# Performance work log

Hardware: AMD Instinct MI355X
Metric: run time of the kernel (lower is better)

## Reference

```python
import jax, jax.numpy as jnp
import numpy as np

HEADS = 16
HEAD_DIM = 64


def _attn(q, k, v):
    # q: [..., Q, h, d], k/v: [..., K, h, d]  (non-causal SDPA, scale 1/sqrt(d))
    scale = 1.0 / np.sqrt(HEAD_DIM).astype(np.float32)
    s = jnp.einsum('...qhd,...khd->...hqk', q, k) * scale
    p = jax.nn.softmax(s, axis=-1)
    return jnp.einsum('...hqk,...khd->...qhd', p, v)


def setup_inputs() -> dict:
    key = jax.random.key(0)
    k0, k1, k2 = jax.random.split(key, 3)
    B, T, H, W, D = 4, 32, 16, 16, 1024
    inner = HEADS * HEAD_DIM
    x = jax.random.normal(k0, (B, T, H, W, D), jnp.float32)
    Wqkv = jax.random.normal(k1, (D, 3 * inner), jnp.float32) / np.sqrt(D)
    Wout = jax.random.normal(k2, (inner, D), jnp.float32) / np.sqrt(inner)
    bout = jnp.zeros((D,), jnp.float32)
    return {"x": x, "Wqkv": Wqkv, "Wout": Wout, "bout": bout, "reference_length": 3}


def reference(x, Wqkv, Wout, bout, reference_length):
    B, T, H, W, D = x.shape
    length = reference_length + 1
    n = T // length            # n_frames (chunks)
    S = H * W                  # tokens per frame
    h, d = HEADS, HEAD_DIM

    qkv = jnp.einsum('bthwD,De->bthwe', x, Wqkv)
    q, k, v = jnp.split(qkv, 3, axis=-1)

    def rs(t):  # -> [B, n, length, S, h, d]
        return t.reshape(B, n, length, S, h, d)

    qr, kr, vr = rs(q), rs(k), rs(v)

    # non-last chunks: query = first frame of chunk, keys/values = remaining r frames
    q_pre = qr[:, :-1, 0]                                             # [B, n-1, S, h, d]
    k_pre = kr[:, :-1, 1:].reshape(B, n - 1, reference_length * S, h, d)
    v_pre = vr[:, :-1, 1:].reshape(B, n - 1, reference_length * S, h, d)
    o_pre = _attn(q_pre, k_pre, v_pre).reshape(B, n - 1, H, W, h * d)

    # last chunk: all `length` frames are queries, keys/values = frames 1..length-1
    q_last = qr[:, -1].reshape(B, length * S, h, d)
    k_last = kr[:, -1, 1:].reshape(B, reference_length * S, h, d)
    v_last = vr[:, -1, 1:].reshape(B, reference_length * S, h, d)
    o_last = _attn(q_last, k_last, v_last).reshape(B, length, H, W, h * d)

    o = jnp.concatenate([o_pre, o_last], axis=1)  # [B, n-1+length, H, W, inner]
    return jnp.einsum('bthwe,eD->bthwD', o, Wout) + bout
```

## Files before the change

### kernel.cpp

```cpp
#include <hip/hip_runtime.h>
#include <hip/hip_bf16.h>

typedef __bf16 bf16;
typedef __bf16 bf16x8 __attribute__((ext_vector_type(8)));
typedef float  f32x4  __attribute__((ext_vector_type(4)));
typedef float  f32x4v __attribute__((ext_vector_type(4)));
typedef unsigned int u32x4 __attribute__((ext_vector_type(4)));
typedef unsigned short u16x4 __attribute__((ext_vector_type(4)));

#define DEV __device__ __forceinline__

DEV void gload_lds16(const bf16* g, bf16* l) {
    __builtin_amdgcn_global_load_lds(
        (__attribute__((address_space(1))) void*)g,
        (__attribute__((address_space(3))) void*)l, 16, 0, 0);
}

DEV bf16x8 as_bf(u32x4 v) { return __builtin_bit_cast(bf16x8, v); }

DEV f32x4 mfma16(bf16x8 a, bf16x8 b, f32x4 c) {
    return __builtin_amdgcn_mfma_f32_16x16x32_bf16(a, b, c, 0, 0, 0);
}

DEV int cvtpk(float lo, float hi) {
    int r;
    asm("v_cvt_pk_bf16_f32 %0, %1, %2" : "=v"(r) : "v"(lo), "v"(hi));
    return r;
}

constexpr int D_   = 1024;
constexpr int S_   = 256;
constexpr int TOUT = 11;
constexpr int MQ   = 4 * TOUT * S_;
constexpr int MKV  = 4 * 8 * 3 * S_;
constexpr int KVL  = 768;

constexpr int PB_WQKV = 768;
constexpr int PB_WOUT = 256;
constexpr int PB_GQ   = MQ  * 128 / 256;
constexpr int PB_GKV  = MKV * 128 / 256;
constexpr int PB_TOT  = PB_WQKV + PB_WOUT + PB_GQ + PB_GKV;

__global__ void prep(const float* __restrict__ x,
                     const float* __restrict__ Wqkv,
                     const float* __restrict__ Wout,
                     bf16* __restrict__ Aq, bf16* __restrict__ Akv,
                     bf16* __restrict__ Wqkv_t, bf16* __restrict__ Wout_t)
{
    __shared__ float T[64][65];
    const int tid = threadIdx.x;
    int wg = blockIdx.x;

    if (wg < PB_WQKV + PB_WOUT) {
        const float* W; bf16* Wt; int N, bid2;
        if (wg < PB_WQKV) { W = Wqkv; Wt = Wqkv_t; N = 3072; bid2 = wg; }
        else              { W = Wout; Wt = Wout_t; N = 1024; bid2 = wg - PB_WQKV; }
        const int kt = bid2 & 15, nt = bid2 >> 4;
        const int k0 = kt * 64, n0 = nt * 64;
        for (int i = 0; i < 16; ++i) {
            const int e = i * 256 + tid;
            const int kk = e >> 6, nn = e & 63;
            T[nn][kk] = W[(size_t)(k0 + kk) * N + n0 + nn];
        }
        __syncthreads();
        for (int i = 0; i < 16; ++i) {
            const int e = i * 256 + tid;
            const int n = e >> 6, kk = e & 63;
            Wt[(size_t)(n0 + n) * 1024 + k0 + kk] = (bf16)T[n][kk];
        }
        return;
    }
    wg -= PB_WQKV + PB_WOUT;

    int row, part;
    const float* src;
    bf16* dst;
    if (wg < PB_GQ) {
        const int idx = wg * 256 + tid;
        row = idx >> 7; part = idx & 127;
        const int b    = row / (TOUT * S_);
        const int r2   = row - b * (TOUT * S_);
        const int tout = r2 >> 8;
        const int s    = r2 & 255;
        const int tx   = tout < 7 ? tout * 4 : 28 + (tout - 7);
        src = x + ((size_t)((b * 32 + tx) * S_ + s)) * D_ + part * 8;
        dst = Aq + (size_t)row * D_ + part * 8;
    } else {
        const int idx = (wg - PB_GQ) * 256 + tid;
        row = idx >> 7; part = idx & 127;
        const int b  = row / 6144;
        const int r2 = row - b * 6144;
        const int c  = r2 / KVL;
        const int j  = r2 - c * KVL;
        const int f  = 1 + (j >> 8);
        const int s  = j & 255;
        const int tx = c * 4 + f;
        src = x + ((size_t)((b * 32 + tx) * S_ + s)) * D_ + part * 8;
        dst = Akv + (size_t)row * D_ + part * 8;
    }
    f32x4v v0 = *(const f32x4v*)src;
    f32x4v v1 = *(const f32x4v*)(src + 4);
    bf16x8 o;
    o[0]=(bf16)v0[0]; o[1]=(bf16)v0[1]; o[2]=(bf16)v0[2]; o[3]=(bf16)v0[3];
    o[4]=(bf16)v1[0]; o[5]=(bf16)v1[1]; o[6]=(bf16)v1[2]; o[7]=(bf16)v1[3];
    *(bf16x8*)dst = o;
}

#define PH_MID() do { \
    __builtin_amdgcn_s_barrier(); \
    asm volatile("s_waitcnt lgkmcnt(0)" ::: "memory"); \
    __builtin_amdgcn_sched_barrier(0); \
    __builtin_amdgcn_s_setprio(1); \
} while(0)

#define PH_END() do { \
    __builtin_amdgcn_s_setprio(0); \
    __builtin_amdgcn_sched_barrier(0); \
    __builtin_amdgcn_s_barrier(); \
} while(0)

#define VM6() asm volatile("s_waitcnt vmcnt(6)" ::: "memory")

#define STAGE_A(bufc, half, tile) do { \
    const bf16* s0_ = pA + (size_t)(half) * 64 * 1024 + (tile) * 64; \
    bf16* d0_ = ldsA + (bufc) * 16384 + (half) * 8192; \
    gload_lds16(s0_, d0_); \
    gload_lds16(s0_ + (size_t)128 * 1024, d0_ + 4096); \
} while(0)

#define STAGE_B(bufc, half, tile) do { \
    const bf16* s0_ = pB + (size_t)(half) * 32 * 1024 + (tile) * 64; \
    bf16* d0_ = ldsB + (bufc) * 16384 + (half) * 8192; \
    gload_lds16(s0_, d0_); \
    gload_lds16(s0_ + (size_t)128 * 1024, d0_ + 4096); \
} while(0)

#define LDA(bufc, mh) do { \
    const bf16* p_ = sm + (bufc) * 16384 + (mh) * 8192; \
    _Pragma("unroll") \
    for (int j_ = 0; j_ < 4; ++j_) { \
        a[j_][0] = *(const u32x4*)(p_ + j_ * 1024 + eA0); \
        a[j_][1] = *(const u32x4*)(p_ + j_ * 1024 + eA1); \
    } \
} while(0)

#define LDB(bufc, nh) do { \
    const bf16* p_ = sm + 32768 + (bufc) * 16384 + (nh) * 8192; \
    _Pragma("unroll") \
    for (int j_ = 0; j_ < 2; ++j_) { \
        b[(nh)*2 + j_][0] = *(const u32x4*)(p_ + j_ * 1024 + eB0); \
        b[(nh)*2 + j_][1] = *(const u32x4*)(p_ + j_ * 1024 + eB1); \
    } \
} while(0)

#define MM(mh, nh) do { \
    _Pragma("unroll") \
    for (int j_ = 0; j_ < 4; ++j_) { \
        _Pragma("unroll") \
        for (int i_ = 0; i_ < 2; ++i_) { \
            f32x4 c_ = acc[(mh)*4 + j_][(nh)*2 + i_]; \
            c_ = mfma16(as_bf(a[j_][0]), as_bf(b[(nh)*2 + i_][0]), c_); \
            c_ = mfma16(as_bf(a[j_][1]), as_bf(b[(nh)*2 + i_][1]), c_); \
            acc[(mh)*4 + j_][(nh)*2 + i_] = c_; \
        } \
    } \
} while(0)

#define GEMM_MAINLOOP() \
    STAGE_A(0, 0, 0); STAGE_B(0, 0, 0); STAGE_B(0, 1, 0); STAGE_A(0, 1, 0); \
    STAGE_A(1, 0, 1); STAGE_B(1, 0, 1); STAGE_B(1, 1, 1); \
    asm volatile("s_waitcnt vmcnt(6)" ::: "memory"); \
    __builtin_amdgcn_s_barrier(); \
    _Pragma("unroll 1") \
    for (int t = 0; t < 8; ++t) { \
        const int T1 = 2 * t + 1; \
        const int n0 = (2 * t + 2 < 15) ? 2 * t + 2 : 15; \
        const int n1 = (2 * t + 3 < 15) ? 2 * t + 3 : 15; \
        LDA(0, 0); LDB(0, 0); STAGE_A(1, 1, T1); \
        PH_MID(); MM(0, 0); PH_END(); \
        LDB(0, 1); STAGE_A(0, 0, n0); \
        PH_MID(); MM(0, 1); PH_END(); \
        LDA(0, 1); STAGE_B(0, 0, n0); \
        PH_MID(); MM(1, 0); PH_END(); \
        STAGE_B(0, 1, n0); \
        PH_MID(); MM(1, 1); VM6(); PH_END(); \
        LDA(1, 0); LDB(1, 0); STAGE_A(0, 1, n0); \
        PH_MID(); MM(0, 0); PH_END(); \
        LDB(1, 1); STAGE_A(1, 0, n1); \
        PH_MID(); MM(0, 1); PH_END(); \
        LDA(1, 1); STAGE_B(1, 0, n1); \
        PH_MID(); MM(1, 0); PH_END(); \
        STAGE_B(1, 1, n1); \
        PH_MID(); MM(1, 1); VM6(); PH_END(); \
    } \
    asm volatile("s_waitcnt vmcnt(0)" ::: "memory")

__global__ __launch_bounds__(512) void gemm_qkv(
    const bf16* __restrict__ Aq, const bf16* __restrict__ Akv,
    const bf16* __restrict__ Wt,
    bf16* __restrict__ Qb, bf16* __restrict__ Kb, bf16* __restrict__ Vt)
{
    __shared__ bf16 sm[65536];
    const int tid = threadIdx.x, lane = tid & 63, wid = tid >> 6;

    int wg = blockIdx.x;
    {
        const int xcd = wg & 7, off = wg >> 3;
        wg = xcd * 118 + off;
    }
    const bool isQ = wg < 176;
    const bf16* A;  const bf16* Bt;  int bm, bn;
    if (isQ) { A = Aq;  Bt = Wt;                      bm = wg % 44;  bn = wg / 44; }
    else     { wg -= 176;
               A = Akv; Bt = Wt + (size_t)1024 * 1024; bm = wg % 96;  bn = wg / 96; }

    const int wr = wid >> 2, wc = wid & 3;
    const int l15 = lane & 15, l4 = lane >> 4;

    const int Rrow = (wid << 3) + (lane >> 3);
    const int G    = (lane & 7) ^ (lane >> 3);
    const bf16* pA = A  + (size_t)(bm * 256 + Rrow) * 1024 + G * 8;
    const int wc1 = Rrow >> 5, cc1 = Rrow & 31;
    const bf16* pB = Bt + (size_t)(bn * 256 + wc1 * 64 + cc1) * 1024 + G * 8;
    bf16* ldsA = sm + (wid << 9);
    bf16* ldsB = sm + 32768 + (wid << 9);

    const int g0  = l4 ^ (l15 & 7);
    const int eA0 = wr * 4096 + l15 * 64 + g0 * 8;
    const int eA1 = eA0 ^ 32;
    const int eB0 = wc * 2048 + l15 * 64 + g0 * 8;
    const int eB1 = eB0 ^ 32;

    f32x4 acc[8][4];
    u32x4 a[4][2], b[4][2];
    const f32x4 zf = {0.f, 0.f, 0.f, 0.f};
    #pragma unroll
    for (int m = 0; m < 8; ++m)
        #pragma unroll
        for (int n = 0; n < 4; ++n) acc[m][n] = zf;

    GEMM_MAINLOOP();

    if (isQ || bn < 4) {
        bf16* C = isQ ? Qb : Kb;
        #pragma unroll
        for (int m = 0; m < 8; ++m) {
            const int row = bm * 256 + wr * 128 + m * 16 + l4 * 4;
            #pragma unroll
            for (int n = 0; n < 4; ++n) {
                const int col = bn * 256 + wc * 64 + n * 16 + l15;
                f32x4 v = acc[m][n];
                #pragma unroll
                for (int r = 0; r < 4; ++r)
                    C[(size_t)(row + r) * 1024 + col] = (bf16)v[r];
            }
        }
    } else {
        const int vb = bm / 3;
        const int j0base = (bm % 3) * 256;
        #pragma unroll
        for (int m = 0; m < 8; ++m) {
            const int j0 = j0base + wr * 128 + m * 16 + l4 * 4;
            #pragma unroll
            for (int n = 0; n < 4; ++n) {
                const int colv = (bn - 4) * 256 + wc * 64 + n * 16 + l15;
                f32x4 v = acc[m][n];
                u16x4 pk;
                #pragma unroll
                for (int r = 0; r < 4; ++r) {
                    bf16 t = (bf16)v[r];
                    pk[r] = __builtin_bit_cast(unsigned short, t);
                }
                *(u16x4*)(Vt + ((size_t)vb * 1024 + colv) * KVL + j0) = pk;
            }
        }
    }
}

__global__ __launch_bounds__(512) void gemm_out(
    const bf16* __restrict__ A, const bf16* __restrict__ Bt,
    float* __restrict__ Cf, const float* __restrict__ bias)
{
    __shared__ bf16 sm[65536];
    const int tid = threadIdx.x, lane = tid & 63, wid = tid >> 6;

    int wg = blockIdx.x;
    {
        const int xcd = wg & 7, off = wg >> 3;
        wg = xcd * 22 + off;
    }
    const int bm = wg % 44, bn = wg / 44;
    const int wr = wid >> 2, wc = wid & 3;
    const int l15 = lane & 15, l4 = lane >> 4;

    const int Rrow = (wid << 3) + (lane >> 3);
    const int G    = (lane & 7) ^ (lane >> 3);
    const bf16* pA = A  + (size_t)(bm * 256 + Rrow) * 1024 + G * 8;
    const int wc1 = Rrow >> 5, cc1 = Rrow & 31;
    const bf16* pB = Bt + (size_t)(bn * 256 + wc1 * 64 + cc1) * 1024 + G * 8;
    bf16* ldsA = sm + (wid << 9);
    bf16* ldsB = sm + 32768 + (wid << 9);

    const int g0  = l4 ^ (l15 & 7);
    const int eA0 = wr * 4096 + l15 * 64 + g0 * 8;
    const int eA1 = eA0 ^ 32;
    const int eB0 = wc * 2048 + l15 * 64 + g0 * 8;
    const int eB1 = eB0 ^ 32;

    f32x4 acc[8][4];
    u32x4 a[4][2], b[4][2];
    const f32x4 zf = {0.f, 0.f, 0.f, 0.f};
    #pragma unroll
    for (int m = 0; m < 8; ++m)
        #pragma unroll
        for (int n = 0; n < 4; ++n) acc[m][n] = zf;

    GEMM_MAINLOOP();

    #pragma unroll
    for (int m = 0; m < 8; ++m) {
        const int row = bm * 256 + wr * 128 + m * 16 + l4 * 4;
        #pragma unroll
        for (int n = 0; n < 4; ++n) {
            const int col = bn * 256 + wc * 64 + n * 16 + l15;
            f32x4 v = acc[m][n];
            const float bs = bias[col];
            #pragma unroll
            for (int r = 0; r < 4; ++r)
                Cf[(size_t)(row + r) * 1024 + col] = v[r] + bs;
        }
    }
}

__global__ __launch_bounds__(256, 4) void attn_fwd(
    const bf16* __restrict__ Q, const bf16* __restrict__ K,
    const bf16* __restrict__ Vt, bf16* __restrict__ O)
{
    __shared__ bf16 Kl[2][2][64][32];
    __shared__ bf16 Vl[2][2][64][32];

    const int tid = threadIdx.x, lane = tid & 63, wid = tid >> 6;
    int bid = blockIdx.x;
    const int h = bid & 15; bid >>= 4;
    const int qt = bid % 44, b = bid / 44;
    const int chunk = qt < 28 ? (qt >> 2) : 7;
    const int qrow0 = b * (TOUT * S_) +
                      (qt < 28 ? chunk * S_ + (qt & 3) * 64 : 7 * S_ + (qt - 28) * 64);

    const bf16* kg = K  + ((size_t)(b * 8 + chunk) * KVL) * 1024 + h * 64;
    const bf16* vg = Vt + ((size_t)((b * 8 + chunk) * 16 + h)) * 64 * KVL;

    const int l15 = lane & 15, l4 = lane >> 4;

    const bf16* qp = Q + (size_t)(qrow0 + wid * 16 + l15) * D_ + h * 64 + l4 * 8;
    u32x4 q0, q1;
    {
        bf16x8 t0 = *(const bf16x8*)qp;
        bf16x8 t1 = *(const bf16x8*)(qp + 32);
        #pragma unroll
        for (int j = 0; j < 8; ++j) {
            t0[j] = (bf16)((float)t0[j] * 0.125f);
            t1[j] = (bf16)((float)t1[j] * 0.125f);
        }
        q0 = __builtin_bit_cast(u32x4, t0);
        q1 = __builtin_bit_cast(u32x4, t1);
    }

    const int R   = wid * 16 + (lane >> 2);
    const int gsw = ((lane & 3) ^ ((lane >> 3) & 3)) * 8;
    const int rg  = (l4 ^ ((l15 >> 1) & 3)) * 8;

    const int baseA = ((2 * (l4 & 1)) * 16 + l15) * 4;
    const int baseB = baseA + 64;
    const bool hi2 = (l4 & 2) != 0;

    float m_s = -1e30f, l_s = 0.f;
    f32x4 oacc[4];
    const f32x4 zf = {0.f, 0.f, 0.f, 0.f};
    #pragma unroll
    for (int m2 = 0; m2 < 4; ++m2) oacc[m2] = zf;

#define ASTAGE(c, t) do { \
    const int kv0_ = (t) * 64; \
    gload_lds16(kg + (size_t)(kv0_ + R) * 1024 + gsw,      &Kl[c][0][0][0] + wid * 512); \
    gload_lds16(kg + (size_t)(kv0_ + R) * 1024 + 32 + gsw, &Kl[c][1][0][0] + wid * 512); \
    gload_lds16(vg + (size_t)R * KVL + kv0_ + gsw,         &Vl[c][0][0][0] + wid * 512); \
    gload_lds16(vg + (size_t)R * KVL + kv0_ + 32 + gsw,    &Vl[c][1][0][0] + wid * 512); \
} while (0)

    ASTAGE(0, 0);
    __syncthreads();

    #pragma unroll 1
    for (int kt = 0; kt < 12; ++kt) {
        const int cur = kt & 1;
        if (kt < 11) ASTAGE(cur ^ 1, kt + 1);

        f32x4 s[4];
        #pragma unroll
        for (int n = 0; n < 4; ++n) {
            const bf16* kp = &Kl[cur][0][n * 16 + l15][0] + rg;
            const u32x4 k0 = *(const u32x4*)kp;
            const u32x4 k1 = *(const u32x4*)(kp + 2048);
            f32x4 t = mfma16(as_bf(k0), as_bf(q0), zf);
            s[n] = mfma16(as_bf(k1), as_bf(q1), t);
        }

        float pm = s[0][0];
        #pragma unroll
        for (int n = 0; n < 4; ++n)
            #pragma unroll
            for (int r = 0; r < 4; ++r) pm = fmaxf(pm, s[n][r]);
        pm = fmaxf(pm, __shfl_xor(pm, 16));
        pm = fmaxf(pm, __shfl_xor(pm, 32));
        const float mn = fmaxf(m_s, pm);
        const float al = __expf(m_s - mn);
        m_s = mn;
        float p[4][4];
        float sum = 0.f;
        #pragma unroll
        for (int n = 0; n < 4; ++n)
            #pragma unroll
            for (int r = 0; r < 4; ++r) {
                const float e = __expf(s[n][r] - mn);
                p[n][r] = e; sum += e;
            }
        sum += __shfl_xor(sum, 16);
        sum += __shfl_xor(sum, 32);
        l_s = l_s * al + sum;
        #pragma unroll
        for (int m2 = 0; m2 < 4; ++m2) oacc[m2] *= al;

        int u[4][2];
        #pragma unroll
        for (int n = 0; n < 4; ++n) {
            u[n][0] = cvtpk(p[n][0], p[n][1]);
            u[n][1] = cvtpk(p[n][2], p[n][3]);
        }

        #pragma unroll
        for (int kk = 0; kk < 2; ++kk) {
            const int e0 = __builtin_amdgcn_ds_bpermute(baseA, u[2 * kk][0]);
            const int f0 = __builtin_amdgcn_ds_bpermute(baseA, u[2 * kk + 1][0]);
            const int e1 = __builtin_amdgcn_ds_bpermute(baseA, u[2 * kk][1]);
            const int f1 = __builtin_amdgcn_ds_bpermute(baseA, u[2 * kk + 1][1]);
            const int e2 = __builtin_amdgcn_ds_bpermute(baseB, u[2 * kk][0]);
            const int f2 = __builtin_amdgcn_ds_bpermute(baseB, u[2 * kk + 1][0]);
            const int e3 = __builtin_amdgcn_ds_bpermute(baseB, u[2 * kk][1]);
            const int f3 = __builtin_amdgcn_ds_bpermute(baseB, u[2 * kk + 1][1]);
            u32x4 pb;
            pb[0] = (unsigned)(hi2 ? f0 : e0);
            pb[1] = (unsigned)(hi2 ? f1 : e1);
            pb[2] = (unsigned)(hi2 ? f2 : e2);
            pb[3] = (unsigned)(hi2 ? f3 : e3);
            #pragma unroll
            for (int m2 = 0; m2 < 4; ++m2) {
                const u32x4 vf = *(const u32x4*)(&Vl[cur][kk][m2 * 16 + l15][0] + rg);
                oacc[m2] = mfma16(as_bf(vf), as_bf(pb), oacc[m2]);
            }
        }
        __syncthreads();
    }
#undef ASTAGE

    const float inv = 1.f / l_s;
    bf16* sc = &Kl[0][0][0][0] + wid * 1152;
    #pragma unroll
    for (int m2 = 0; m2 < 4; ++m2)
        #pragma unroll
        for (int r = 0; r < 4; ++r)
            sc[l15 * 72 + m2 * 16 + l4 * 4 + r] = (bf16)(oacc[m2][r] * inv);
    const int rq = lane >> 2, rd = (lane & 3) * 16;
    const bf16* sr = sc + rq * 72 + rd;
    const u32x4 o0 = *(const u32x4*)sr;
    const u32x4 o1 = *(const u32x4*)(sr + 8);
    bf16* op = O + (size_t)(qrow0 + wid * 16 + rq) * D_ + h * 64 + rd;
    *(u32x4*)op = o0;
    *(u32x4*)(op + 8) = o1;
}

extern "C" void kernel_launch(void* const* d_in, const int* in_sizes, int n_in,
                              void* d_out, int out_size, void* d_ws, size_t ws_size,
                              hipStream_t stream) {
    (void)in_sizes; (void)n_in; (void)out_size; (void)ws_size;
    const float* x    = (const float*)d_in[0];
    const float* Wqkv = (const float*)d_in[1];
    const float* Wout = (const float*)d_in[2];
    const float* bout = (const float*)d_in[3];

    bf16* Aq     = (bf16*)d_ws;
    bf16* Akv    = Aq     + (size_t)MQ  * 1024;
    bf16* Wqkv_t = Akv    + (size_t)MKV * 1024;
    bf16* Wout_t = Wqkv_t + (size_t)3072 * 1024;
    bf16* Qb     = Wout_t + (size_t)1024 * 1024;
    bf16* Kb     = Qb     + (size_t)MQ  * 1024;
    bf16* Vtb    = Kb     + (size_t)MKV * 1024;
    bf16* Ob     = Aq;

    prep<<<PB_TOT, 256, 0, stream>>>(x, Wqkv, Wout, Aq, Akv, Wqkv_t, Wout_t);

    gemm_qkv<<<944, 512, 0, stream>>>(Aq, Akv, Wqkv_t, Qb, Kb, Vtb);

    attn_fwd<<<4 * 44 * 16, 256, 0, stream>>>(Qb, Kb, Vtb, Ob);

    gemm_out<<<176, 512, 0, stream>>>(Ob, Wout_t, (float*)d_out, bout);
}
```

Baseline: 308.4 us.

## Software-pipeline LDS fragment reads across MFMA phases with double-buffered registers

Restructures the GEMM main loop so the LDS-to-register fragment loads for the next MFMA phase are issued right after the current phase's MFMAs, into alternate register sets (aX/aY, bP/bQ), instead of being loaded just before use. This is meant to hide LDS read latency behind MFMA execution and reduce stalls at each phase barrier. It also sets launch_bounds occupancy hints of 2 blocks per CU and moves the vmcnt wait into every phase close, which raises register pressure and may force tighter allocation or spills.

```diff
diff --git a/kernel.cpp b/kernel.cpp
--- a/kernel.cpp
+++ b/kernel.cpp
@@ -106,20 +106,22 @@
     *(bf16x8*)dst = o;
 }
 
-#define PH_MID() do { \
+#define PH_BEGIN() do { \
     __builtin_amdgcn_s_barrier(); \
     asm volatile("s_waitcnt lgkmcnt(0)" ::: "memory"); \
     __builtin_amdgcn_sched_barrier(0); \
     __builtin_amdgcn_s_setprio(1); \
 } while(0)
 
-#define PH_END() do { \
+#define PH_MMEND() do { \
     __builtin_amdgcn_s_setprio(0); \
     __builtin_amdgcn_sched_barrier(0); \
+} while(0)
+
+#define PH_CLOSE() do { \
+    asm volatile("s_waitcnt vmcnt(6)" ::: "memory"); \
     __builtin_amdgcn_s_barrier(); \
 } while(0)
-
-#define VM6() asm volatile("s_waitcnt vmcnt(6)" ::: "memory")
 
 #define STAGE_A(bufc, half, tile) do { \
     const bf16* s0_ = pA + (size_t)(half) * 64 * 1024 + (tile) * 64; \
@@ -135,67 +137,105 @@
     gload_lds16(s0_ + (size_t)128 * 1024, d0_ + 4096); \
 } while(0)
 
-#define LDA(bufc, mh) do { \
-    const bf16* p_ = sm + (bufc) * 16384 + (mh) * 8192; \
-    _Pragma("unroll") \
-    for (int j_ = 0; j_ < 4; ++j_) { \
-        a[j_][0] = *(const u32x4*)(p_ + j_ * 1024 + eA0); \
-        a[j_][1] = *(const u32x4*)(p_ + j_ * 1024 + eA1); \
-    } \
-} while(0)
-
-#define LDB(bufc, nh) do { \
+#define LDAJ(dst, bufc, mh, J) do { \
+    const bf16* p_ = sm + (bufc) * 16384 + (mh) * 8192 + (J) * 1024; \
+    dst[J][0] = *(const u32x4*)(p_ + eA0); \
+    dst[J][1] = *(const u32x4*)(p_ + eA1); \
+} while(0)
+
+#define LDBH(dst, bufc, nh) do { \
     const bf16* p_ = sm + 32768 + (bufc) * 16384 + (nh) * 8192; \
-    _Pragma("unroll") \
-    for (int j_ = 0; j_ < 2; ++j_) { \
-        b[(nh)*2 + j_][0] = *(const u32x4*)(p_ + j_ * 1024 + eB0); \
-        b[(nh)*2 + j_][1] = *(const u32x4*)(p_ + j_ * 1024 + eB1); \
-    } \
-} while(0)
-
-#define MM(mh, nh) do { \
+    dst[0][0] = *(const u32x4*)(p_ + eB0); \
+    dst[0][1] = *(const u32x4*)(p_ + eB1); \
+    dst[1][0] = *(const u32x4*)(p_ + 1024 + eB0); \
+    dst[1][1] = *(const u32x4*)(p_ + 1024 + eB1); \
+} while(0)
+
+#define MMX(av, bv, mh, nh) do { \
     _Pragma("unroll") \
     for (int j_ = 0; j_ < 4; ++j_) { \
         _Pragma("unroll") \
         for (int i_ = 0; i_ < 2; ++i_) { \
             f32x4 c_ = acc[(mh)*4 + j_][(nh)*2 + i_]; \
-            c_ = mfma16(as_bf(a[j_][0]), as_bf(b[(nh)*2 + i_][0]), c_); \
-            c_ = mfma16(as_bf(a[j_][1]), as_bf(b[(nh)*2 + i_][1]), c_); \
+            c_ = mfma16(as_bf(av[j_][0]), as_bf(bv[i_][0]), c_); \
+            c_ = mfma16(as_bf(av[j_][1]), as_bf(bv[i_][1]), c_); \
             acc[(mh)*4 + j_][(nh)*2 + i_] = c_; \
         } \
     } \
 } while(0)
 
-#define GEMM_MAINLOOP() \
-    STAGE_A(0, 0, 0); STAGE_B(0, 0, 0); STAGE_B(0, 1, 0); STAGE_A(0, 1, 0); \
+#define GEMM_MAINLOOP() do { \
+    STAGE_A(0, 0, 0); STAGE_A(0, 1, 0); STAGE_B(0, 0, 0); STAGE_B(0, 1, 0); \
     STAGE_A(1, 0, 1); STAGE_B(1, 0, 1); STAGE_B(1, 1, 1); \
     asm volatile("s_waitcnt vmcnt(6)" ::: "memory"); \
     __builtin_amdgcn_s_barrier(); \
+    LDAJ(aX,0,0,0); LDAJ(aX,0,0,1); LDAJ(aX,0,0,2); LDAJ(aX,0,0,3); \
+    LDBH(bP,0,0); \
     _Pragma("unroll 1") \
     for (int t = 0; t < 8; ++t) { \
         const int T1 = 2 * t + 1; \
         const int n0 = (2 * t + 2 < 15) ? 2 * t + 2 : 15; \
         const int n1 = (2 * t + 3 < 15) ? 2 * t + 3 : 15; \
-        LDA(0, 0); LDB(0, 0); STAGE_A(1, 1, T1); \
-        PH_MID(); MM(0, 0); PH_END(); \
-        LDB(0, 1); STAGE_A(0, 0, n0); \
-        PH_MID(); MM(0, 1); PH_END(); \
-        LDA(0, 1); STAGE_B(0, 0, n0); \
-        PH_MID(); MM(1, 0); PH_END(); \
+        STAGE_A(1, 1, T1); \
+        PH_BEGIN(); MMX(aX, bP, 0, 0); PH_MMEND(); \
+        LDBH(bQ, 0, 1); LDAJ(aY, 0, 1, 0); \
+        PH_CLOSE(); \
+        STAGE_A(0, 0, n0); \
+        PH_BEGIN(); MMX(aX, bQ, 0, 1); PH_MMEND(); \
+        LDAJ(aY, 0, 1, 1); LDAJ(aY, 0, 1, 2); LDAJ(aY, 0, 1, 3); \
+        PH_CLOSE(); \
+        STAGE_B(0, 0, n0); \
+        PH_BEGIN(); MMX(aY, bP, 1, 0); PH_MMEND(); \
+        LDAJ(aX, 1, 0, 0); LDAJ(aX, 1, 0, 1); LDAJ(aX, 1, 0, 2); \
+        PH_CLOSE(); \
         STAGE_B(0, 1, n0); \
-        PH_MID(); MM(1, 1); VM6(); PH_END(); \
-        LDA(1, 0); LDB(1, 0); STAGE_A(0, 1, n0); \
-        PH_MID(); MM(0, 0); PH_END(); \
-        LDB(1, 1); STAGE_A(1, 0, n1); \
-        PH_MID(); MM(0, 1); PH_END(); \
-        LDA(1, 1); STAGE_B(1, 0, n1); \
-        PH_MID(); MM(1, 0); PH_END(); \
+        PH_BEGIN(); MMX(aY, bQ, 1, 1); PH_MMEND(); \
+        LDAJ(aX, 1, 0, 3); LDBH(bP, 1, 0); \
+        PH_CLOSE(); \
+        STAGE_A(0, 1, n0); \
+        PH_BEGIN(); MMX(aX, bP, 0, 0); PH_MMEND(); \
+        LDBH(bQ, 1, 1); LDAJ(aY, 1, 1, 0); \
+        PH_CLOSE(); \
+        STAGE_A(1, 0, n1); \
+        PH_BEGIN(); MMX(aX, bQ, 0, 1); PH_MMEND(); \
+        LDAJ(aY, 1, 1, 1); LDAJ(aY, 1, 1, 2); LDAJ(aY, 1, 1, 3); \
+        PH_CLOSE(); \
+        STAGE_B(1, 0, n1); \
+        PH_BEGIN(); MMX(aY, bP, 1, 0); PH_MMEND(); \
+        LDAJ(aX, 0, 0, 0); LDAJ(aX, 0, 0, 1); LDAJ(aX, 0, 0, 2); \
+        PH_CLOSE(); \
         STAGE_B(1, 1, n1); \
-        PH_MID(); MM(1, 1); VM6(); PH_END(); \
+        PH_BEGIN(); MMX(aY, bQ, 1, 1); PH_MMEND(); \
+        LDAJ(aX, 0, 0, 3); LDBH(bP, 0, 0); \
+        PH_CLOSE(); \
     } \
-    asm volatile("s_waitcnt vmcnt(0)" ::: "memory")
-
-__global__ __launch_bounds__(512) void gemm_qkv(
+    asm volatile("s_waitcnt vmcnt(0) lgkmcnt(0)" ::: "memory"); \
+} while(0)
+
+#define GEMM_PREAMBLE() \
+    const int wr = wid >> 2, wc = wid & 3; \
+    const int l15 = lane & 15, l4 = lane >> 4; \
+    const int Rrow = (wid << 3) + (lane >> 3); \
+    const int G    = (lane & 7) ^ (lane >> 3); \
+    const bf16* pA = A  + (size_t)(bm * 256 + Rrow) * 1024 + G * 8; \
+    const int wc1 = Rrow >> 5, cc1 = Rrow & 31; \
+    const bf16* pB = Bt + (size_t)(bn * 256 + wc1 * 64 + cc1) * 1024 + G * 8; \
+    bf16* ldsA = sm + (wid << 9); \
+    bf16* ldsB = sm + 32768 + (wid << 9); \
+    const int g0  = l4 ^ (l15 & 7); \
+    const int eA0 = wr * 4096 + l15 * 64 + g0 * 8; \
+    const int eA1 = eA0 ^ 32; \
+    const int eB0 = wc * 2048 + l15 * 64 + g0 * 8; \
+    const int eB1 = eB0 ^ 32; \
+    f32x4 acc[8][4]; \
+    u32x4 aX[4][2], aY[4][2], bP[2][2], bQ[2][2]; \
+    { const f32x4 zf_ = {0.f, 0.f, 0.f, 0.f}; \
+      _Pragma("unroll") \
+      for (int m_ = 0; m_ < 8; ++m_) \
+          _Pragma("unroll") \
+          for (int n_ = 0; n_ < 4; ++n_) acc[m_][n_] = zf_; }
+
+__global__ __launch_bounds__(512, 2) void gemm_qkv(
     const bf16* __restrict__ Aq, const bf16* __restrict__ Akv,
     const bf16* __restrict__ Wt,
     bf16* __restrict__ Qb, bf16* __restrict__ Kb, bf16* __restrict__ Vt)
@@ -210,35 +250,11 @@
     }
     const bool isQ = wg < 176;
     const bf16* A;  const bf16* Bt;  int bm, bn;
-    if (isQ) { A = Aq;  Bt = Wt;                      bm = wg % 44;  bn = wg / 44; }
+    if (isQ) { A = Aq;  Bt = Wt;                       bm = wg % 44;  bn = wg / 44; }
     else     { wg -= 176;
                A = Akv; Bt = Wt + (size_t)1024 * 1024; bm = wg % 96;  bn = wg / 96; }
 
-    const int wr = wid >> 2, wc = wid & 3;
-    const int l15 = lane & 15, l4 = lane >> 4;
-
-    const int Rrow = (wid << 3) + (lane >> 3);
-    const int G    = (lane & 7) ^ (lane >> 3);
-    const bf16* pA = A  + (size_t)(bm * 256 + Rrow) * 1024 + G * 8;
-    const int wc1 = Rrow >> 5, cc1 = Rrow & 31;
-    const bf16* pB = Bt + (size_t)(bn * 256 + wc1 * 64 + cc1) * 1024 + G * 8;
-    bf16* ldsA = sm + (wid << 9);
-    bf16* ldsB = sm + 32768 + (wid << 9);
-
-    const int g0  = l4 ^ (l15 & 7);
-    const int eA0 = wr * 4096 + l15 * 64 + g0 * 8;
-    const int eA1 = eA0 ^ 32;
-    const int eB0 = wc * 2048 + l15 * 64 + g0 * 8;
-    const int eB1 = eB0 ^ 32;
-
-    f32x4 acc[8][4];
-    u32x4 a[4][2], b[4][2];
-    const f32x4 zf = {0.f, 0.f, 0.f, 0.f};
-    #pragma unroll
-    for (int m = 0; m < 8; ++m)
-        #pragma unroll
-        for (int n = 0; n < 4; ++n) acc[m][n] = zf;
-
+    GEMM_PREAMBLE();
     GEMM_MAINLOOP();
 
     if (isQ || bn < 4) {
@@ -277,7 +293,7 @@
     }
 }
 
-__global__ __launch_bounds__(512) void gemm_out(
+__global__ __launch_bounds__(512, 2) void gemm_out(
     const bf16* __restrict__ A, const bf16* __restrict__ Bt,
     float* __restrict__ Cf, const float* __restrict__ bias)
 {
@@ -290,31 +306,8 @@
         wg = xcd * 22 + off;
     }
     const int bm = wg % 44, bn = wg / 44;
-    const int wr = wid >> 2, wc = wid & 3;
-    const int l15 = lane & 15, l4 = lane >> 4;
-
-    const int Rrow = (wid << 3) + (lane >> 3);
-    const int G    = (lane & 7) ^ (lane >> 3);
-    const bf16* pA = A  + (size_t)(bm * 256 + Rrow) * 1024 + G * 8;
-    const int wc1 = Rrow >> 5, cc1 = Rrow & 31;
-    const bf16* pB = Bt + (size_t)(bn * 256 + wc1 * 64 + cc1) * 1024 + G * 8;
-    bf16* ldsA = sm + (wid << 9);
-    bf16* ldsB = sm + 32768 + (wid << 9);
-
-    const int g0  = l4 ^ (l15 & 7);
-    const int eA0 = wr * 4096 + l15 * 64 + g0 * 8;
-    const int eA1 = eA0 ^ 32;
-    const int eB0 = wc * 2048 + l15 * 64 + g0 * 8;
-    const int eB1 = eB0 ^ 32;
-
-    f32x4 acc[8][4];
-    u32x4 a[4][2], b[4][2];
-    const f32x4 zf = {0.f, 0.f, 0.f, 0.f};
-    #pragma unroll
-    for (int m = 0; m < 8; ++m)
-        #pragma unroll
-        for (int n = 0; n < 4; ++n) acc[m][n] = zf;
-
+
+    GEMM_PREAMBLE();
     GEMM_MAINLOOP();
 
     #pragma unroll
```

New measurement: 309.0 us (median of 4 runs). No clear change (+0.2%).
